# Kernel tuning notes

Hardware: AMD Instinct MI355X
Metric: run time of the kernel (lower is better)

The kernel has to match this reference:

```python
import jax, jax.numpy as jnp
import numpy as np
import math

B, T, C, H = 4, 1024, 1024, 16
D = C // H  # head dim = 64

def setup_inputs() -> dict:
    key = jax.random.key(0)
    ks = jax.random.split(key, 10)
    s = 1.0 / math.sqrt(C)
    x = jax.random.normal(ks[0], (B, T, C), dtype=jnp.float32)
    pad = (jax.random.uniform(ks[1], (B, T)) < 0.2).astype(jnp.float32)
    # ensure first token of every row is unpadded so softmax rows are well-posed
    pad = pad.at[:, 0].set(0.0)
    Wq = jax.random.normal(ks[2], (C, C), dtype=jnp.float32) * s
    bq = jnp.zeros((C,), dtype=jnp.float32)
    Wk = jax.random.normal(ks[3], (C, C), dtype=jnp.float32) * s
    bk = jnp.zeros((C,), dtype=jnp.float32)
    Wv = jax.random.normal(ks[4], (C, C), dtype=jnp.float32) * s
    bv = jnp.zeros((C,), dtype=jnp.float32)
    Wp = jax.random.normal(ks[5], (C, C), dtype=jnp.float32) * s
    bp = jnp.zeros((C,), dtype=jnp.float32)
    return {"x": x, "x_padding_judge": pad, "Wq": Wq, "bq": bq,
            "Wk": Wk, "bk": bk, "Wv": Wv, "bv": bv, "Wp": Wp, "bp": bp}

def reference(x, x_padding_judge, Wq, bq, Wk, bk, Wv, bv, Wp, bp):
    # keep flag: 1.0 where token is real, 0.0 where padded
    keep = 1.0 - x_padding_judge                      # [B, T]
    mask = keep[:, :, None] * keep[:, None, :]        # [B, T, T] outer product
    # projections, split heads: [B, H, T, D]
    def heads(w, b):
        return (x @ w + b).reshape(B, T, H, D).transpose(0, 2, 1, 3)
    q, k, v = heads(Wq, bq), heads(Wk, bk), heads(Wv, bv)
    att = jnp.einsum('bhqd,bhkd->bhqk', q, k) * (1.0 / math.sqrt(D))
    # attn_pdrop=0 => att_full is all ones; masked_fill where mask == 0
    att = jnp.where(mask[:, None, :, :] == 0, -1e9, att)
    att = jax.nn.softmax(att, axis=-1)
    y = jnp.einsum('bhqk,bhkd->bhqd', att, v)         # [B, H, T, D]
    y = y.transpose(0, 2, 1, 3).reshape(B, T, C)
    return y @ Wp + bp
```

## Files before the change

kernel.cpp:

```cpp
#include <hip/hip_runtime.h>
#include <hip/hip_bf16.h>
#include <math.h>

#define Bb 4
#define Tt 1024
#define Cc 1024
#define Hh 16
#define Dd 64

typedef __attribute__((ext_vector_type(8))) _Float16 half8;
typedef __attribute__((ext_vector_type(4))) _Float16 half4;
typedef __attribute__((ext_vector_type(4))) float floatx4;


__device__ __forceinline__ void gload_lds16(const _Float16* g, const _Float16* l)
{
    __builtin_amdgcn_global_load_lds(
        (const __attribute__((address_space(1))) void*)g,
        (__attribute__((address_space(3))) void*)l, 16, 0, 0);
}

struct PrepP { const float* x; _Float16* xh; const float* W[4]; _Float16* out[4]; };

__global__ __launch_bounds__(256) void prep_all(PrepP p)
{
    if (blockIdx.x < 256) {
        const int m16 = blockIdx.x;
        const int r   = threadIdx.x & 15;
        const int kc0 = threadIdx.x >> 4;
        const float* src = p.x + (size_t)(m16 * 16 + r) * 1024;
        _Float16*   dst = p.xh + (size_t)m16 * 16384 + r * 8;
#pragma unroll
        for (int c8 = 0; c8 < 8; ++c8) {
            const int kc = kc0 + c8 * 16;
            float4 a = *(const float4*)(src + kc * 8);
            float4 b = *(const float4*)(src + kc * 8 + 4);
            half8 h;
            h[0] = (_Float16)a.x; h[1] = (_Float16)a.y; h[2] = (_Float16)a.z; h[3] = (_Float16)a.w;
            h[4] = (_Float16)b.x; h[5] = (_Float16)b.y; h[6] = (_Float16)b.z; h[7] = (_Float16)b.w;
            *(half8*)(dst + kc * 128) = h;
        }
        return;
    }
    const int bid2 = blockIdx.x - 256;
    const int z    = bid2 >> 8;
    const int rem  = bid2 & 255;
    const int n0   = (rem & 15) * 64;
    const int k0   = (rem >> 4) * 64;
    const float* __restrict__ W = p.W[z];
    _Float16* __restrict__ outp = p.out[z];
    __shared__ float tile[64][65];
    const int tr  = threadIdx.x >> 4;
    const int tc4 = (threadIdx.x & 15) * 4;

#pragma unroll
    for (int i = 0; i < 4; ++i) {
        const int kk = tr + i * 16;
        float4 v = *(const float4*)(W + (size_t)(k0 + kk) * 1024 + n0 + tc4);
        tile[kk][tc4 + 0] = v.x;
        tile[kk][tc4 + 1] = v.y;
        tile[kk][tc4 + 2] = v.z;
        tile[kk][tc4 + 3] = v.w;
    }
    __syncthreads();
#pragma unroll
    for (int i = 0; i < 4; ++i) {
        half4 h;
#pragma unroll
        for (int c = 0; c < 4; ++c) h[c] = (_Float16)tile[tc4 + c][tr + i * 16];
        _Float16* dst = outp + (size_t)((n0 >> 4) + i) * 16384
                        + ((k0 + tc4) >> 3) * 128 + tr * 8 + (tc4 & 7);
        *(half4*)dst = h;
    }
}

struct QkvP { const _Float16* Wt[3]; const float* bias[3];
              _Float16* qb; _Float16* kb; _Float16* vt; };

#define QKV_STEP(CUR, SBUF, TS, DOSTAGE, TAILWAIT)                          \
    {                                                                       \
        half8 af[2], bf[4];                                                 \
        _Pragma("unroll")                                                   \
        for (int i = 0; i < 2; ++i)                                         \
            af[i] = *(const half8*)&As[CUR][wr * 2 + i][lane * 8];          \
        _Pragma("unroll")                                                   \
        for (int j = 0; j < 4; ++j)                                         \
            bf[j] = *(const half8*)&Bs[CUR][wc * 4 + j][lane * 8];          \
        if (DOSTAGE) {                                                      \
            const size_t ko = (size_t)(TS) * 512;                           \
            gload_lds16(ga + ko, &As[SBUF][w][0]);                          \
            gload_lds16(gb + ko, &Bs[SBUF][w][0]);                          \
        }                                                                   \
        _Pragma("unroll")                                                   \
        for (int i = 0; i < 2; ++i)                                         \
            _Pragma("unroll")                                               \
            for (int j = 0; j < 4; ++j)                                     \
                acc[i][j] = __builtin_amdgcn_mfma_f32_16x16x32_f16(         \
                    af[i], bf[j], acc[i][j], 0, 0, 0);                      \
        if ((TAILWAIT) == 2)                                                \
            asm volatile("s_waitcnt vmcnt(2)" ::: "memory");                \
        else if ((TAILWAIT) == 0)                                           \
            asm volatile("s_waitcnt vmcnt(0)" ::: "memory");                \
        if ((TAILWAIT) >= 0) __builtin_amdgcn_s_barrier();                  \
    }

__global__ __launch_bounds__(512) void gemm_qkv(const _Float16* __restrict__ xh, QkvP p)
{
    const int z = blockIdx.z;
    const _Float16* __restrict__ Wt   = p.Wt[z];
    const float* __restrict__    bias = p.bias[z];

    const int tid  = threadIdx.x;
    const int lane = tid & 63;
    const int w    = tid >> 6;
    const int wr   = w >> 1, wc = w & 1;
    const int quad = lane >> 4;
    const int l15  = lane & 15;
    const int bm   = blockIdx.x * 128;
    const int bn   = blockIdx.y * 128;

    __shared__ __align__(16) _Float16 As[3][8][512];
    __shared__ __align__(16) _Float16 Bs[3][8][512];

    const _Float16* ga = xh + (size_t)((bm >> 4) + w) * 16384 + lane * 8;
    const _Float16* gb = Wt + (size_t)((bn >> 4) + w) * 16384 + lane * 8;

    floatx4 acc[2][4];
#pragma unroll
    for (int i = 0; i < 2; ++i)
#pragma unroll
        for (int j = 0; j < 4; ++j)
            acc[i][j] = (floatx4){0.f, 0.f, 0.f, 0.f};

    gload_lds16(ga, &As[0][w][0]);
    gload_lds16(gb, &Bs[0][w][0]);
    gload_lds16(ga + 512, &As[1][w][0]);
    gload_lds16(gb + 512, &Bs[1][w][0]);
    asm volatile("s_waitcnt vmcnt(2)" ::: "memory");
    __builtin_amdgcn_s_barrier();

    for (int tt = 0; tt < 30; tt += 3) {
        QKV_STEP(0, 2, tt + 2, true, 2);
        QKV_STEP(1, 0, tt + 3, true, 2);
        QKV_STEP(2, 1, tt + 4, true, 2);
    }
    QKV_STEP(0, 0, 0, false, 0);
    QKV_STEP(1, 0, 0, false, -1);

    if (z == 2) {
#pragma unroll
        for (int j = 0; j < 4; ++j) {
            const int col = bn + wc * 64 + j * 16 + l15;
            const int h  = col >> 6;
            const float bj = bias[col];
#pragma unroll
            for (int i = 0; i < 2; ++i) {
                const int t0 = bm + wr * 32 + i * 16 + quad * 4;
                const int bh = (t0 >> 10) * 16 + h;
                const int tm = t0 & 1023;
                half4 pk;
#pragma unroll
                for (int r = 0; r < 4; ++r) pk[r] = (_Float16)(acc[i][j][r] + bj);
                *(half4*)(p.vt + (size_t)bh * 65536 + (size_t)j * 16384
                          + (tm >> 3) * 128 + l15 * 8 + (tm & 7)) = pk;
            }
        }
    } else {
        _Float16* outp = (z == 0) ? p.qb : p.kb;
#pragma unroll
        for (int j = 0; j < 4; ++j) {
            const int col = bn + wc * 64 + j * 16 + l15;
            const int h  = col >> 6;
            const int dd = col & 63;
            const float bj = bias[col];
            const int doff = (dd >> 3) * 128 + (dd & 7);
#pragma unroll
            for (int i = 0; i < 2; ++i) {
#pragma unroll
                for (int r = 0; r < 4; ++r) {
                    const int tg = bm + wr * 32 + i * 16 + quad * 4 + r;
                    const int bh = (tg >> 10) * 16 + h;
                    const int tm = tg & 1023;
                    outp[(size_t)bh * 65536 + (tm >> 4) * 1024 + doff + (tm & 15) * 8] =
                        (_Float16)(acc[i][j][r] + bj);
                }
            }
        }
    }
}

__global__ __launch_bounds__(256) void attn_mfma(
    const _Float16* __restrict__ qb, const _Float16* __restrict__ kb,
    const _Float16* __restrict__ vt, const float* __restrict__ padj,
    _Float16* __restrict__ yh)
{
    __shared__ __align__(16) _Float16 Ps[4][2048];

    const int tid  = threadIdx.x;
    const int lane = tid & 63;
    const int w    = tid >> 6;
    const int quad = lane >> 4;
    const int l15  = lane & 15;
    const int bh   = blockIdx.x;
    const int q0   = blockIdx.y * 128;
    const int b    = bh >> 4;
    const int h    = bh & 15;

    const _Float16* qf = qb + (size_t)bh * 65536;
    const _Float16* kf = kb + (size_t)bh * 65536;
    const _Float16* vf = vt + (size_t)bh * 65536;
    const float*    pk_row = padj + b * Tt;

    half8 bq[2][2];
#pragma unroll
    for (int ks = 0; ks < 2; ++ks)
#pragma unroll
        for (int nq = 0; nq < 2; ++nq)
            bq[ks][nq] = *(const half8*)(qf + (size_t)((q0 >> 4) + w * 2 + nq) * 1024
                                         + ks * 512 + lane * 8);
    float kq[2];
#pragma unroll
    for (int nq = 0; nq < 2; ++nq)
        kq[nq] = 1.0f - pk_row[q0 + w * 32 + nq * 16 + l15];

    floatx4 O[2][4];
    floatx4 l_acc[2];
#pragma unroll
    for (int mi = 0; mi < 2; ++mi) {
#pragma unroll
        for (int dj = 0; dj < 4; ++dj) O[mi][dj] = (floatx4){0.f, 0.f, 0.f, 0.f};
        l_acc[mi] = (floatx4){0.f, 0.f, 0.f, 0.f};
    }
    half8 ones;
#pragma unroll
    for (int j = 0; j < 8; ++j) ones[j] = (_Float16)1.0f;

    constexpr float SC = 0.18033688011112042f;

    for (int kt = 0; kt < Tt; kt += 64) {
        half8 ak[2][4], bv[2][4];
#pragma unroll
        for (int ks = 0; ks < 2; ++ks)
#pragma unroll
            for (int mk = 0; mk < 4; ++mk)
                ak[ks][mk] = *(const half8*)(kf + (size_t)((kt >> 4) + mk) * 1024
                                             + ks * 512 + lane * 8);
#pragma unroll
        for (int ks = 0; ks < 2; ++ks)
#pragma unroll
            for (int dj = 0; dj < 4; ++dj)
                bv[ks][dj] = *(const half8*)(vf + (size_t)dj * 16384 + (kt >> 3) * 128
                                             + ks * 512 + lane * 8);
        float4 kk4[4];
#pragma unroll
        for (int mk = 0; mk < 4; ++mk)
            kk4[mk] = *(const float4*)(pk_row + kt + mk * 16 + quad * 4);

        floatx4 ST[4][2];
#pragma unroll
        for (int mk = 0; mk < 4; ++mk)
#pragma unroll
            for (int nq = 0; nq < 2; ++nq)
                ST[mk][nq] = (floatx4){0.f, 0.f, 0.f, 0.f};
#pragma unroll
        for (int ks = 0; ks < 2; ++ks)
#pragma unroll
            for (int mk = 0; mk < 4; ++mk)
#pragma unroll
                for (int nq = 0; nq < 2; ++nq)
                    ST[mk][nq] = __builtin_amdgcn_mfma_f32_16x16x32_f16(
                        ak[ks][mk], bq[ks][nq], ST[mk][nq], 0, 0, 0);

#pragma unroll
        for (int mk = 0; mk < 4; ++mk) {
            const float kkr[4] = {1.0f - kk4[mk].x, 1.0f - kk4[mk].y,
                                  1.0f - kk4[mk].z, 1.0f - kk4[mk].w};
#pragma unroll
            for (int nq = 0; nq < 2; ++nq) {
                half4 pk;
#pragma unroll
                for (int r = 0; r < 4; ++r) {
                    const float e = __builtin_amdgcn_exp2f(ST[mk][nq][r] * SC);
                    const float pv = (kq[nq] == 0.0f) ? 1.0f : kkr[r] * e;
                    pk[r] = (_Float16)pv;
                }
                *(half4*)&Ps[w][((mk * 2 + (quad >> 1)) * 32 + nq * 16 + l15) * 8
                               + (quad & 1) * 4] = pk;
            }
        }

#pragma unroll
        for (int ks = 0; ks < 2; ++ks) {
            half8 ap[2];
#pragma unroll
            for (int mi = 0; mi < 2; ++mi)
                ap[mi] = *(const half8*)&Ps[w][((ks * 4 + quad) * 32 + mi * 16 + l15) * 8];
#pragma unroll
            for (int mi = 0; mi < 2; ++mi) {
#pragma unroll
                for (int dj = 0; dj < 4; ++dj)
                    O[mi][dj] = __builtin_amdgcn_mfma_f32_16x16x32_f16(
                        ap[mi], bv[ks][dj], O[mi][dj], 0, 0, 0);
                l_acc[mi] = __builtin_amdgcn_mfma_f32_16x16x32_f16(
                    ap[mi], ones, l_acc[mi], 0, 0, 0);
            }
        }
    }

#pragma unroll
    for (int mi = 0; mi < 2; ++mi) {
#pragma unroll
        for (int r = 0; r < 4; ++r) {
            const int rowl  = w * 32 + mi * 16 + quad * 4 + r;
            const int token = b * Tt + q0 + rowl;
            const float inv = 1.0f / l_acc[mi][r];
            const size_t tb = (size_t)(token >> 4) * 16384 + (token & 15) * 8;
#pragma unroll
            for (int dj = 0; dj < 4; ++dj) {
                const int col = h * 64 + dj * 16 + l15;
                yh[tb + (col >> 3) * 128 + (col & 7)] = (_Float16)(O[mi][dj][r] * inv);
            }
        }
    }
}

#define PROJ_STEP(CUR, SBUF, TS, DOSTAGE, TAILWAIT)                         \
    {                                                                       \
        half8 af[2], bf[4];                                                 \
        _Pragma("unroll")                                                   \
        for (int i = 0; i < 2; ++i)                                         \
            af[i] = *(const half8*)&As[CUR][wr * 2 + i][lane * 8];          \
        _Pragma("unroll")                                                   \
        for (int j = 0; j < 4; ++j)                                         \
            bf[j] = *(const half8*)&Bs[CUR][wc * 4 + j][lane * 8];          \
        if (DOSTAGE) {                                                      \
            const size_t ko = (size_t)(TS) * 512;                           \
            gload_lds16(ga + ko, &As[SBUF][w][0]);                          \
            gload_lds16(gb + ko, &Bs[SBUF][w][0]);                          \
        }                                                                   \
        _Pragma("unroll")                                                   \
        for (int i = 0; i < 2; ++i)                                         \
            _Pragma("unroll")                                               \
            for (int j = 0; j < 4; ++j)                                     \
                acc[i][j] = __builtin_amdgcn_mfma_f32_16x16x32_f16(         \
                    af[i], bf[j], acc[i][j], 0, 0, 0);                      \
        if ((TAILWAIT) == 6)                                                \
            asm volatile("s_waitcnt vmcnt(6)" ::: "memory");                \
        else if ((TAILWAIT) == 4)                                           \
            asm volatile("s_waitcnt vmcnt(4)" ::: "memory");                \
        else if ((TAILWAIT) == 2)                                           \
            asm volatile("s_waitcnt vmcnt(2)" ::: "memory");                \
        else if ((TAILWAIT) == 0)                                           \
            asm volatile("s_waitcnt vmcnt(0)" ::: "memory");                \
        if ((TAILWAIT) >= 0) __builtin_amdgcn_s_barrier();                  \
    }

__global__ __launch_bounds__(512) void gemm_proj(const _Float16* __restrict__ Ay,
                                                 const _Float16* __restrict__ Bt,
                                                 const float* __restrict__ bias,
                                                 float* __restrict__ out)
{
    const int tid  = threadIdx.x;
    const int lane = tid & 63;
    const int w    = tid >> 6;
    const int wr   = w >> 1, wc = w & 1;
    const int quad = lane >> 4;
    const int l15  = lane & 15;
    const int bm   = blockIdx.x * 128;
    const int bn   = blockIdx.y * 128;

    __shared__ __align__(16) _Float16 As[5][8][512];
    __shared__ __align__(16) _Float16 Bs[5][8][512];

    const _Float16* ga = Ay + (size_t)((bm >> 4) + w) * 16384 + lane * 8;
    const _Float16* gb = Bt + (size_t)((bn >> 4) + w) * 16384 + lane * 8;

    floatx4 acc[2][4];
#pragma unroll
    for (int i = 0; i < 2; ++i)
#pragma unroll
        for (int j = 0; j < 4; ++j)
            acc[i][j] = (floatx4){0.f, 0.f, 0.f, 0.f};

#pragma unroll
    for (int tb = 0; tb < 4; ++tb) {
        gload_lds16(ga + (size_t)tb * 512, &As[tb][w][0]);
        gload_lds16(gb + (size_t)tb * 512, &Bs[tb][w][0]);
    }
    asm volatile("s_waitcnt vmcnt(6)" ::: "memory");
    __builtin_amdgcn_s_barrier();

    for (int tt = 0; tt < 25; tt += 5) {
        PROJ_STEP(0, 4, tt + 4, true, 6);
        PROJ_STEP(1, 0, tt + 5, true, 6);
        PROJ_STEP(2, 1, tt + 6, true, 6);
        PROJ_STEP(3, 2, tt + 7, true, 6);
        PROJ_STEP(4, 3, tt + 8, true, 6);
    }
    PROJ_STEP(0, 4, 29, true, 6);
    PROJ_STEP(1, 0, 30, true, 6);
    PROJ_STEP(2, 1, 31, true, 6);
    PROJ_STEP(3, 0, 0, false, 4);
    PROJ_STEP(4, 0, 0, false, 2);
    PROJ_STEP(0, 0, 0, false, 0);
    PROJ_STEP(1, 0, 0, false, -1);

#pragma unroll
    for (int j = 0; j < 4; ++j) {
        const int col = bn + wc * 64 + j * 16 + l15;
        const float bj = bias[col];
#pragma unroll
        for (int i = 0; i < 2; ++i) {
            const int row = bm + wr * 32 + i * 16 + quad * 4;
            float* o = out + (size_t)row * 1024 + col;
#pragma unroll
            for (int r = 0; r < 4; ++r)
                o[(size_t)r * 1024] = acc[i][j][r] + bj;
        }
    }
}

extern "C" void kernel_launch(void* const* d_in, const int* in_sizes, int n_in,
                              void* d_out, int out_size, void* d_ws, size_t ws_size,
                              hipStream_t stream)
{
    const float* x    = (const float*)d_in[0];
    const float* padj = (const float*)d_in[1];
    const float* Wq   = (const float*)d_in[2];
    const float* bq   = (const float*)d_in[3];
    const float* Wk   = (const float*)d_in[4];
    const float* bk   = (const float*)d_in[5];
    const float* Wv   = (const float*)d_in[6];
    const float* bv   = (const float*)d_in[7];
    const float* Wp   = (const float*)d_in[8];
    const float* bp   = (const float*)d_in[9];
    float* out = (float*)d_out;

    const size_t MB = 1024 * 1024;
    char* ws = (char*)d_ws;
    _Float16* xh  = (_Float16*)(ws);
    _Float16* Wt0 = (_Float16*)(ws +  8 * MB);
    _Float16* Wt1 = (_Float16*)(ws + 10 * MB);
    _Float16* Wt2 = (_Float16*)(ws + 12 * MB);
    _Float16* Wtp = (_Float16*)(ws + 14 * MB);
    _Float16* qb  = (_Float16*)(ws + 16 * MB);
    _Float16* kb  = (_Float16*)(ws + 24 * MB);
    _Float16* vtb = (_Float16*)(ws + 32 * MB);
    _Float16* yh  = (_Float16*)(ws + 40 * MB);

    PrepP pp;
    pp.x = x; pp.xh = xh;
    pp.W[0] = Wq; pp.W[1] = Wk; pp.W[2] = Wv; pp.W[3] = Wp;
    pp.out[0] = Wt0; pp.out[1] = Wt1; pp.out[2] = Wt2; pp.out[3] = Wtp;
    prep_all<<<1280, 256, 0, stream>>>(pp);

    QkvP qp;
    qp.Wt[0] = Wt0; qp.Wt[1] = Wt1; qp.Wt[2] = Wt2;
    qp.bias[0] = bq; qp.bias[1] = bk; qp.bias[2] = bv;
    qp.qb = qb; qp.kb = kb; qp.vt = vtb;
    gemm_qkv<<<dim3(32, 8, 3), 512, 0, stream>>>(xh, qp);

    attn_mfma<<<dim3(64, 8), 256, 0, stream>>>(qb, kb, vtb, padj, yh);

    gemm_proj<<<dim3(32, 8), 512, 0, stream>>>(yh, Wtp, bp, out);
}
```

Measured before the change: 176.5 us.

## Stage K/V tiles through triple-buffered LDS with async global-to-LDS loads

The attention kernel no longer has each of the four waves fetch K and V fragments straight from global memory. The block now cooperatively loads each 64-key K/V tile into a three-deep LDS ring buffer with global_load_lds, prefetching two tiles ahead, using explicit vmcnt waits and barriers. The padding row is also copied into LDS once. The aim is to remove the duplicated global traffic across waves and hide load latency behind the MFMA and exp work. The cost is more LDS use, which may lower occupancy, plus a barrier on every step.

```diff
diff --git a/kernel.cpp b/kernel.cpp
--- a/kernel.cpp
+++ b/kernel.cpp
@@ -189,12 +189,97 @@
     }
 }
 
+#define ATTN_STEP(CUR, SBUF, TC, TS, DOSTAGE, TAILWAIT)                     \
+    {                                                                       \
+        half8 ak[2][4], bv[2][4];                                           \
+        _Pragma("unroll")                                                   \
+        for (int ks = 0; ks < 2; ++ks)                                      \
+            _Pragma("unroll")                                               \
+            for (int mk = 0; mk < 4; ++mk)                                  \
+                ak[ks][mk] = *(const half8*)&Ks[CUR][mk * 2 + ks][lane * 8];\
+        _Pragma("unroll")                                                   \
+        for (int ks = 0; ks < 2; ++ks)                                      \
+            _Pragma("unroll")                                               \
+            for (int dj = 0; dj < 4; ++dj)                                  \
+                bv[ks][dj] = *(const half8*)&Vs[CUR][dj * 2 + ks][lane * 8];\
+        if (DOSTAGE) {                                                      \
+            _Pragma("unroll")                                               \
+            for (int c = 0; c < 2; ++c) {                                   \
+                const int f = w * 2 + c;                                    \
+                gload_lds16(kf + (size_t)((TS) * 4 + (f >> 1)) * 1024       \
+                            + (f & 1) * 512 + lane * 8, &Ks[SBUF][f][0]);   \
+                gload_lds16(vf + (size_t)(f >> 1) * 16384                   \
+                            + (size_t)(TS) * 1024 + (f & 1) * 512           \
+                            + lane * 8, &Vs[SBUF][f][0]);                   \
+            }                                                               \
+        }                                                                   \
+        float4 kk4[4];                                                      \
+        _Pragma("unroll")                                                   \
+        for (int mk = 0; mk < 4; ++mk)                                      \
+            kk4[mk] = *(const float4*)&Pad[(TC) * 64 + mk * 16 + quad * 4]; \
+        floatx4 ST[4][2];                                                   \
+        _Pragma("unroll")                                                   \
+        for (int mk = 0; mk < 4; ++mk)                                      \
+            _Pragma("unroll")                                               \
+            for (int nq = 0; nq < 2; ++nq)                                  \
+                ST[mk][nq] = (floatx4){0.f, 0.f, 0.f, 0.f};                 \
+        _Pragma("unroll")                                                   \
+        for (int ks = 0; ks < 2; ++ks)                                      \
+            _Pragma("unroll")                                               \
+            for (int mk = 0; mk < 4; ++mk)                                  \
+                _Pragma("unroll")                                           \
+                for (int nq = 0; nq < 2; ++nq)                              \
+                    ST[mk][nq] = __builtin_amdgcn_mfma_f32_16x16x32_f16(    \
+                        ak[ks][mk], bq[ks][nq], ST[mk][nq], 0, 0, 0);       \
+        _Pragma("unroll")                                                   \
+        for (int mk = 0; mk < 4; ++mk) {                                    \
+            const float kkr[4] = {1.0f - kk4[mk].x, 1.0f - kk4[mk].y,       \
+                                  1.0f - kk4[mk].z, 1.0f - kk4[mk].w};      \
+            _Pragma("unroll")                                               \
+            for (int nq = 0; nq < 2; ++nq) {                                \
+                half4 pk;                                                   \
+                _Pragma("unroll")                                           \
+                for (int r = 0; r < 4; ++r) {                               \
+                    const float e = __builtin_amdgcn_exp2f(ST[mk][nq][r] * SC); \
+                    const float pv = (kq[nq] == 0.0f) ? 1.0f : kkr[r] * e;  \
+                    pk[r] = (_Float16)pv;                                   \
+                }                                                           \
+                *(half4*)&Ps[w][((mk * 2 + (quad >> 1)) * 32 + nq * 16 + l15) * 8 \
+                               + (quad & 1) * 4] = pk;                      \
+            }                                                               \
+        }                                                                   \
+        _Pragma("unroll")                                                   \
+        for (int ks = 0; ks < 2; ++ks) {                                    \
+            half8 ap[2];                                                    \
+            _Pragma("unroll")                                               \
+            for (int mi = 0; mi < 2; ++mi)                                  \
+                ap[mi] = *(const half8*)&Ps[w][((ks * 4 + quad) * 32 + mi * 16 + l15) * 8]; \
+            _Pragma("unroll")                                               \
+            for (int mi = 0; mi < 2; ++mi) {                                \
+                _Pragma("unroll")                                           \
+                for (int dj = 0; dj < 4; ++dj)                              \
+                    O[mi][dj] = __builtin_amdgcn_mfma_f32_16x16x32_f16(     \
+                        ap[mi], bv[ks][dj], O[mi][dj], 0, 0, 0);            \
+                l_acc[mi] = __builtin_amdgcn_mfma_f32_16x16x32_f16(         \
+                    ap[mi], ones, l_acc[mi], 0, 0, 0);                      \
+            }                                                               \
+        }                                                                   \
+        if ((TAILWAIT) == 4)                                                \
+            asm volatile("s_waitcnt vmcnt(4)" ::: "memory");                \
+        else if ((TAILWAIT) == 0)                                           \
+            asm volatile("s_waitcnt vmcnt(0)" ::: "memory");                \
+        if ((TAILWAIT) >= 0) __builtin_amdgcn_s_barrier();                  \
+    }
+
 __global__ __launch_bounds__(256) void attn_mfma(
     const _Float16* __restrict__ qb, const _Float16* __restrict__ kb,
     const _Float16* __restrict__ vt, const float* __restrict__ padj,
     _Float16* __restrict__ yh)
 {
     __shared__ __align__(16) _Float16 Ps[4][2048];
+    __shared__ __align__(16) _Float16 Ks[3][8][512];
+    __shared__ __align__(16) _Float16 Vs[3][8][512];
+    __shared__ __align__(16) float    Pad[1024];
 
     const int tid  = threadIdx.x;
     const int lane = tid & 63;
@@ -211,6 +296,8 @@
     const _Float16* vf = vt + (size_t)bh * 65536;
     const float*    pk_row = padj + b * Tt;
 
+    *(float4*)&Pad[tid * 4] = *(const float4*)(pk_row + tid * 4);
+
     half8 bq[2][2];
 #pragma unroll
     for (int ks = 0; ks < 2; ++ks)
@@ -237,75 +324,31 @@
 
     constexpr float SC = 0.18033688011112042f;
 
-    for (int kt = 0; kt < Tt; kt += 64) {
-        half8 ak[2][4], bv[2][4];
-#pragma unroll
-        for (int ks = 0; ks < 2; ++ks)
-#pragma unroll
-            for (int mk = 0; mk < 4; ++mk)
-                ak[ks][mk] = *(const half8*)(kf + (size_t)((kt >> 4) + mk) * 1024
-                                             + ks * 512 + lane * 8);
-#pragma unroll
-        for (int ks = 0; ks < 2; ++ks)
-#pragma unroll
-            for (int dj = 0; dj < 4; ++dj)
-                bv[ks][dj] = *(const half8*)(vf + (size_t)dj * 16384 + (kt >> 3) * 128
-                                             + ks * 512 + lane * 8);
-        float4 kk4[4];
-#pragma unroll
-        for (int mk = 0; mk < 4; ++mk)
-            kk4[mk] = *(const float4*)(pk_row + kt + mk * 16 + quad * 4);
-
-        floatx4 ST[4][2];
-#pragma unroll
-        for (int mk = 0; mk < 4; ++mk)
-#pragma unroll
-            for (int nq = 0; nq < 2; ++nq)
-                ST[mk][nq] = (floatx4){0.f, 0.f, 0.f, 0.f};
-#pragma unroll
-        for (int ks = 0; ks < 2; ++ks)
-#pragma unroll
-            for (int mk = 0; mk < 4; ++mk)
-#pragma unroll
-                for (int nq = 0; nq < 2; ++nq)
-                    ST[mk][nq] = __builtin_amdgcn_mfma_f32_16x16x32_f16(
-                        ak[ks][mk], bq[ks][nq], ST[mk][nq], 0, 0, 0);
-
-#pragma unroll
-        for (int mk = 0; mk < 4; ++mk) {
-            const float kkr[4] = {1.0f - kk4[mk].x, 1.0f - kk4[mk].y,
-                                  1.0f - kk4[mk].z, 1.0f - kk4[mk].w};
-#pragma unroll
-            for (int nq = 0; nq < 2; ++nq) {
-                half4 pk;
-#pragma unroll
-                for (int r = 0; r < 4; ++r) {
-                    const float e = __builtin_amdgcn_exp2f(ST[mk][nq][r] * SC);
-                    const float pv = (kq[nq] == 0.0f) ? 1.0f : kkr[r] * e;
-                    pk[r] = (_Float16)pv;
-                }
-                *(half4*)&Ps[w][((mk * 2 + (quad >> 1)) * 32 + nq * 16 + l15) * 8
-                               + (quad & 1) * 4] = pk;
-            }
+    __syncthreads();
+
+#pragma unroll
+    for (int tb = 0; tb < 2; ++tb) {
+#pragma unroll
+        for (int c = 0; c < 2; ++c) {
+            const int f = w * 2 + c;
+            gload_lds16(kf + (size_t)(tb * 4 + (f >> 1)) * 1024
+                        + (f & 1) * 512 + lane * 8, &Ks[tb][f][0]);
+            gload_lds16(vf + (size_t)(f >> 1) * 16384 + (size_t)tb * 1024
+                        + (f & 1) * 512 + lane * 8, &Vs[tb][f][0]);
         }
-
-#pragma unroll
-        for (int ks = 0; ks < 2; ++ks) {
-            half8 ap[2];
-#pragma unroll
-            for (int mi = 0; mi < 2; ++mi)
-                ap[mi] = *(const half8*)&Ps[w][((ks * 4 + quad) * 32 + mi * 16 + l15) * 8];
-#pragma unroll
-            for (int mi = 0; mi < 2; ++mi) {
-#pragma unroll
-                for (int dj = 0; dj < 4; ++dj)
-                    O[mi][dj] = __builtin_amdgcn_mfma_f32_16x16x32_f16(
-                        ap[mi], bv[ks][dj], O[mi][dj], 0, 0, 0);
-                l_acc[mi] = __builtin_amdgcn_mfma_f32_16x16x32_f16(
-                    ap[mi], ones, l_acc[mi], 0, 0, 0);
-            }
-        }
-    }
+    }
+    asm volatile("s_waitcnt vmcnt(4)" ::: "memory");
+    __builtin_amdgcn_s_barrier();
+
+    for (int tt = 0; tt < 12; tt += 3) {
+        ATTN_STEP(0, 2, tt + 0, tt + 2, true, 4);
+        ATTN_STEP(1, 0, tt + 1, tt + 3, true, 4);
+        ATTN_STEP(2, 1, tt + 2, tt + 4, true, 4);
+    }
+    ATTN_STEP(0, 2, 12, 14, true, 4);
+    ATTN_STEP(1, 0, 13, 15, true, 4);
+    ATTN_STEP(2, 0, 14, 0, false, 0);
+    ATTN_STEP(0, 0, 15, 0, false, -1);
 
 #pragma unroll
     for (int mi = 0; mi < 2; ++mi) {
```

Result: no change. 177.7 us (+0.6%).
